# Optimization experiments

Measured on AMD Instinct MI355X. Metric: run time of the kernel, lower is better.

## Reference

```python
import jax, jax.numpy as jnp
import numpy as np
from jax import lax

EPS = 1e-5

def _conv(x, w, b, pad):
    y = lax.conv_general_dilated(x, w, (1, 1), [(pad, pad), (pad, pad)],
                                 dimension_numbers=('NCHW', 'OIHW', 'NCHW'))
    return y + b[None, :, None, None]

def _bn(x, g, b, m, v):
    # eval-mode BatchNorm2d with running stats
    scale = g * lax.rsqrt(v + EPS)
    return x * scale[None, :, None, None] + (b - m * scale)[None, :, None, None]

def setup_inputs() -> dict:
    key = jax.random.key(0)
    ks = jax.random.split(key, 16)
    B, C, H, W = 16, 64, 128, 128
    C2 = 2 * C
    d = {}
    d['x'] = jax.random.normal(ks[0], (B, C, H, W), jnp.float32)
    # fc1: Conv2d(C,C,3,p=1) + BN(C)
    d['fc1_w'] = jax.random.normal(ks[1], (C, C, 3, 3), jnp.float32) * 0.05
    d['fc1_b'] = jax.random.normal(ks[2], (C,), jnp.float32) * 0.05
    d['bn1_g'] = jnp.ones((C,), jnp.float32)
    d['bn1_b'] = jnp.zeros((C,), jnp.float32)
    d['bn1_m'] = jax.random.normal(ks[3], (C,), jnp.float32) * 0.05
    d['bn1_v'] = jax.random.uniform(ks[4], (C,), jnp.float32) * 0.5 + 0.5
    # graph_conv.nn: Conv2d(2C,2C,1) + BN(2C) + GELU
    d['gc_w'] = jax.random.normal(ks[5], (C2, C2, 1, 1), jnp.float32) * 0.05
    d['gc_b'] = jax.random.normal(ks[6], (C2,), jnp.float32) * 0.05
    d['bng_g'] = jnp.ones((C2,), jnp.float32)
    d['bng_b'] = jnp.zeros((C2,), jnp.float32)
    d['bng_m'] = jax.random.normal(ks[7], (C2,), jnp.float32) * 0.05
    d['bng_v'] = jax.random.uniform(ks[8], (C2,), jnp.float32) * 0.5 + 0.5
    # fc2: Conv2d(2C,C,3,p=1) + BN(C)
    d['fc2_w'] = jax.random.normal(ks[9], (C, C2, 3, 3), jnp.float32) * 0.05
    d['fc2_b'] = jax.random.normal(ks[10], (C,), jnp.float32) * 0.05
    d['bn2_g'] = jnp.ones((C,), jnp.float32)
    d['bn2_b'] = jnp.zeros((C,), jnp.float32)
    d['bn2_m'] = jax.random.normal(ks[11], (C,), jnp.float32) * 0.05
    d['bn2_v'] = jax.random.uniform(ks[12], (C,), jnp.float32) * 0.5 + 0.5
    return d

def reference(x, fc1_w, fc1_b, bn1_g, bn1_b, bn1_m, bn1_v,
              gc_w, gc_b, bng_g, bng_b, bng_m, bng_v,
              fc2_w, fc2_b, bn2_g, bn2_b, bn2_m, bn2_v):
    # fc1
    h = _bn(_conv(x, fc1_w, fc1_b, 1), bn1_g, bn1_b, bn1_m, bn1_v)
    # MRConv4dSP: strided self-attention over superpatch tokens
    sel = h[:, :, ::4, ::4]                          # [B,C,h4,w4]
    B, C, h4, w4 = sel.shape
    q = sel.reshape(B, C, h4 * w4).transpose(0, 2, 1)  # [B,N,C]
    scale = C ** (-0.5)
    att = jax.nn.softmax(jnp.einsum('bnc,bmc->bnm', q, q) * scale, axis=-1)
    o = jnp.einsum('bnm,bmc->bnc', att, q)           # [B,N,C]
    o = o.transpose(0, 2, 1).reshape(B, C, h4, w4)
    o = jnp.repeat(jnp.repeat(o, 4, axis=2), 4, axis=3)
    g = jnp.concatenate([h, o], axis=1)              # [B,2C,H,W]
    g = jax.nn.gelu(_bn(_conv(g, gc_w, gc_b, 0), bng_g, bng_b, bng_m, bng_v),
                    approximate=False)
    # fc2 + residual (drop_path=0 -> identity)
    y = _bn(_conv(g, fc2_w, fc2_b, 1), bn2_g, bn2_b, bn2_m, bn2_v)
    return y + x
```

## Files before the change

### kernel.cpp

```cpp
#include <hip/hip_runtime.h>
#include <math.h>

#define EPSV 1e-5f

typedef __bf16 bf16;
using bf16x8 = __attribute__((ext_vector_type(8))) __bf16;
using bf16x4 = __attribute__((ext_vector_type(4))) __bf16;
using bf16x2 = __attribute__((ext_vector_type(2))) __bf16;
using f32x4  = __attribute__((ext_vector_type(4))) float;

static __device__ __forceinline__ f32x4 mfma16(bf16x8 a, bf16x8 b, f32x4 c) {
    return __builtin_amdgcn_mfma_f32_16x16x32_bf16(a, b, c, 0, 0, 0);
}
static __device__ __forceinline__ f32x4 zero4() {
    f32x4 z = {0.f, 0.f, 0.f, 0.f};
    return z;
}

typedef __attribute__((address_space(1))) const char g_char_t;
typedef __attribute__((address_space(3))) char lds_char_t;
static __device__ __forceinline__ void gll16(const void* g, void* l) {
    __builtin_amdgcn_global_load_lds((g_char_t*)g, (lds_char_t*)l, 16, 0, 0);
}

static __device__ __forceinline__ float gelu_f(float v) {
    float z = fabsf(v) * 0.70710678118f;
    float t = __builtin_amdgcn_rcpf(1.f + 0.3275911f * z);
    float poly = t * (0.254829592f + t * (-0.284496736f + t * (1.421413741f +
                 t * (-1.453152027f + t * 1.061405429f))));
    float e = __expf(-z * z);
    float erfv = copysignf(1.f - poly * e, v);
    return 0.5f * v * (1.f + erfv);
}

static __device__ __forceinline__ void prep3x3_one(const float* w, bf16* wt,
                                                   int t, int CIN)
{
    int cout = t / CIN, ci = t - cout * CIN;
    int cci = ci >> 5, lg = (ci >> 3) & 3, j = ci & 7;
    int mi = cout >> 4, lix = cout & 15;
#pragma unroll
    for (int kgt = 0; kgt < 9; ++kgt) {
        float v = w[(size_t)t * 9 + kgt];
        wt[((((size_t)kgt * (CIN >> 5) + cci) * 4 + mi) * 64 + lg * 16 + lix) * 8 + j]
            = (bf16)v;
    }
}

__global__ __launch_bounds__(256) void prep_cvt(
    const float* __restrict__ x, bf16* __restrict__ xb,
    const float* __restrict__ fc1_w, const float* __restrict__ fc2_w,
    const float* __restrict__ gc_w,
    bf16* __restrict__ wt1, bf16* __restrict__ wt2, bf16* __restrict__ wtg,
    float* __restrict__ zb)
{
    __shared__ float t_lds[64 * 68];
    const int bx = blockIdx.x, tid = threadIdx.x;
    if (bx < 4096) {
        const int b = bx >> 8, inner = bx & 255;
        const int y = inner >> 1, x0 = (inner & 1) * 64;
        for (int f = tid; f < 64 * 16; f += 256) {
            int c = f >> 4, xu = f & 15;
            float4 v = *(const float4*)&x[((size_t)(b * 64 + c) << 14) + (y << 7) + x0 + xu * 4];
            t_lds[(xu * 4 + 0) * 68 + c] = v.x;
            t_lds[(xu * 4 + 1) * 68 + c] = v.y;
            t_lds[(xu * 4 + 2) * 68 + c] = v.z;
            t_lds[(xu * 4 + 3) * 68 + c] = v.w;
        }
        __syncthreads();
        for (int f = tid; f < 64 * 8; f += 256) {
            int xx = f >> 3, cu = f & 7;
            const float* p = &t_lds[xx * 68 + cu * 8];
            bf16x8 v;
#pragma unroll
            for (int j = 0; j < 8; ++j) v[j] = (bf16)p[j];
            *(bf16x8*)&xb[((size_t)((b * 128 + y) * 128) + x0 + xx) * 64 + cu * 8] = v;
        }
    } else {
        int px = bx - 4096;
        if (px < 16) {
            prep3x3_one(fc1_w, wt1, px * 256 + tid, 64);
        } else if (px < 48) {
            prep3x3_one(fc2_w, wt2, (px - 16) * 256 + tid, 128);
        } else {
            if (px == 48 && tid < 64)
                ((float4*)zb)[tid] = make_float4(0.f, 0.f, 0.f, 0.f);
            int t = (px - 48) * 256 + tid;
            int cout = t >> 7, ci = t & 127;
            int ks = ci >> 5, lg = (ci >> 3) & 3, j = ci & 7;
            wtg[(((size_t)(ks * 4 + lg) * 128) + cout) * 8 + j] = (bf16)gc_w[t];
        }
    }
}

template<int CIN, int OUTMODE>
__global__ __launch_bounds__(512) void conv3x3_mfma(
    const bf16* __restrict__ in, const bf16* __restrict__ wt,
    const float* __restrict__ bias,
    const float* __restrict__ bg, const float* __restrict__ bb,
    const float* __restrict__ bm, const float* __restrict__ bv,
    const bf16* __restrict__ resid, const bf16* __restrict__ zb,
    void* __restrict__ outp, bf16* __restrict__ qout)
{
    constexpr int NC = CIN >> 5;
    __shared__ bf16 in_lds[2][672 * 32];
    __shared__ bf16 w_lds[2][36 * 512];

    const int wg = blockIdx.x;
    const int v  = (wg & 7) * 64 + (wg >> 3);
    const int tile = v & 31, b = v >> 5;
    const int x0 = (tile & 1) * 64;
    const int y0 = (tile >> 1) * 8;
    const int tid  = threadIdx.x;
    const int wid  = tid >> 6;
    const int lane = tid & 63;
    const int lix  = lane & 15, lg = lane >> 4;

    int goff[6]; bool gok[6];
#pragma unroll
    for (int i = 0; i < 6; ++i) {
        int chunk = wid + 8 * i;
        int f = chunk * 64 + lane;
        int pix = f >> 2, u = f & 3;
        int sw = (pix & 3) ^ ((pix >> 2) & 3);
        int ug = u ^ sw;
        int iy = pix / 66, ix = pix - iy * 66;
        int gy = y0 + iy - 1, gx = x0 + ix - 1;
        gok[i]  = (chunk < 42) && (pix < 660) &&
                  (unsigned)gy < 128u && (unsigned)gx < 128u;
        goff[i] = ((b * 128 + gy) * 128 + gx) * CIN + ug * 8;
    }
    int rd[9];
#pragma unroll
    for (int kg = 0; kg < 3; ++kg)
#pragma unroll
        for (int t = 0; t < 3; ++t) {
            int pix0 = (wid + kg) * 66 + lix + t;
            int sw = (pix0 & 3) ^ ((pix0 >> 2) & 3);
            rd[kg * 3 + t] = pix0 * 32 + ((lg ^ sw) << 3);
        }

    f32x4 acc[4][4];
#pragma unroll
    for (int i = 0; i < 4; ++i)
#pragma unroll
        for (int j = 0; j < 4; ++j) acc[i][j] = zero4();

    auto issue_in = [&](int cci, int buf) {
#pragma unroll
        for (int i = 0; i < 6; ++i) {
            int chunk = wid + 8 * i;
            if (chunk < 42) {
                const void* src = gok[i] ? (const void*)(in + goff[i] + cci * 32)
                                         : (const void*)zb;
                gll16(src, (char*)&in_lds[buf][0] + chunk * 1024);
            }
        }
    };
    auto issue_w = [&](int cci, int buf) {
#pragma unroll
        for (int i = 0; i < 5; ++i) {
            int chunk = wid + 8 * i;
            if (chunk < 36) {
                const bf16* src = wt + ((size_t)(chunk >> 2) * NC + cci) * 2048
                                     + (chunk & 3) * 512 + lane * 8;
                gll16(src, (char*)&w_lds[buf][0] + chunk * 1024);
            }
        }
    };
    auto compute = [&](int buf) {
        bf16x8 afA[4], bfA[4], afB[4], bfB[4];
#pragma unroll
        for (int mi = 0; mi < 4; ++mi)
            afA[mi] = *(const bf16x8*)&w_lds[buf][(0 * 4 + mi) * 512 + lane * 8];
#pragma unroll
        for (int nj = 0; nj < 4; ++nj)
            bfA[nj] = *(const bf16x8*)&in_lds[buf][rd[0] + nj * 512];
#pragma unroll
        for (int kgt = 0; kgt < 9; ++kgt) {
            bf16x8* afC = (kgt & 1) ? afB : afA;
            bf16x8* bfC = (kgt & 1) ? bfB : bfA;
            bf16x8* afN = (kgt & 1) ? afA : afB;
            bf16x8* bfN = (kgt & 1) ? bfA : bfB;
            if (kgt < 8) {
#pragma unroll
                for (int mi = 0; mi < 4; ++mi)
                    afN[mi] = *(const bf16x8*)&w_lds[buf][((kgt + 1) * 4 + mi) * 512 + lane * 8];
#pragma unroll
                for (int nj = 0; nj < 4; ++nj)
                    bfN[nj] = *(const bf16x8*)&in_lds[buf][rd[kgt + 1] + nj * 512];
            }
            __builtin_amdgcn_sched_barrier(0);
#pragma unroll
            for (int nj = 0; nj < 4; ++nj)
#pragma unroll
                for (int mi = 0; mi < 4; ++mi)
                    acc[mi][nj] = mfma16(afC[mi], bfC[nj], acc[mi][nj]);
            __builtin_amdgcn_sched_barrier(0);
        }
    };

    issue_in(0, 0);
    issue_w(0, 0);
#pragma unroll 1
    for (int c = 0; c < NC; ++c) {
        if (c + 1 < NC) {
            issue_in(c + 1, (c + 1) & 1);
            issue_w(c + 1, (c + 1) & 1);
            if (wid < 2)      asm volatile("s_waitcnt vmcnt(11)" ::: "memory");
            else if (wid < 4) asm volatile("s_waitcnt vmcnt(10)" ::: "memory");
            else              asm volatile("s_waitcnt vmcnt(9)"  ::: "memory");
        } else {
            asm volatile("s_waitcnt vmcnt(0)" ::: "memory");
        }
        __builtin_amdgcn_s_barrier();
        __builtin_amdgcn_sched_barrier(0);
        compute(c & 1);
        __builtin_amdgcn_s_barrier();
    }

    if (OUTMODE == 0) {
        bf16* out = (bf16*)outp;
        bf16* stg = &in_lds[0][0];
#pragma unroll
        for (int mi = 0; mi < 4; ++mi) {
            float A[4], Bc[4];
#pragma unroll
            for (int r = 0; r < 4; ++r) {
                int c = mi * 16 + lg * 4 + r;
                float s = bg[c] * rsqrtf(bv[c] + EPSV);
                A[r]  = s;
                Bc[r] = bias[c] * s + bb[c] - bm[c] * s;
            }
#pragma unroll
            for (int nj = 0; nj < 4; ++nj) {
                int px = nj * 16 + lix;
                bf16x4 vv;
#pragma unroll
                for (int r = 0; r < 4; ++r)
                    vv[r] = (bf16)(acc[mi][nj][r] * A[r] + Bc[r]);
                *(bf16x4*)&stg[(wid * 64 + px) * 68 + mi * 16 + lg * 4] = vv;
            }
        }
        __syncthreads();
#pragma unroll
        for (int k = 0; k < 8; ++k) {
            int idx = k * 512 + tid;
            int row = idx >> 9, rem = idx & 511;
            int px = rem >> 3, cu = rem & 7;
            bf16x8 vv = *(const bf16x8*)&stg[(row * 64 + px) * 68 + cu * 8];
            *(bf16x8*)&out[((size_t)((b * 128 + y0 + row) * 128)
                            + x0 + px) * 64 + cu * 8] = vv;
        }
        if (qout && tid < 256) {
            int row4 = (tid >> 7) * 4;
            int rem  = tid & 127;
            int px4  = (rem >> 3) * 4, cu = rem & 7;
            int gy = y0 + row4, gx = x0 + px4;
            int n = ((gy >> 2) << 5) + (gx >> 2);
            bf16x8 vv = *(const bf16x8*)&stg[(row4 * 64 + px4) * 68 + cu * 8];
            *(bf16x8*)&qout[((size_t)(b * 1024 + n)) * 64 + cu * 8] = vv;
        }
    } else {
        float* out = (float*)outp;
        const int gy = y0 + wid;
#pragma unroll
        for (int mi = 0; mi < 4; ++mi) {
            float A[4], Bc[4];
#pragma unroll
            for (int r = 0; r < 4; ++r) {
                int c = mi * 16 + lg * 4 + r;
                float s = bg[c] * rsqrtf(bv[c] + EPSV);
                A[r]  = s;
                Bc[r] = bias[c] * s + bb[c] - bm[c] * s;
            }
#pragma unroll
            for (int nj = 0; nj < 4; ++nj) {
                int px = x0 + nj * 16 + lix;
                bf16x4 rv = *(const bf16x4*)&resid[((size_t)((b * 128 + gy) * 128) + px) * 64
                                                   + mi * 16 + lg * 4];
#pragma unroll
                for (int r = 0; r < 4; ++r) {
                    int c = mi * 16 + lg * 4 + r;
                    size_t oi = ((size_t)(b * 64 + c) << 14) + (gy << 7) + px;
                    out[oi] = acc[mi][nj][r] * A[r] + Bc[r] + (float)rv[r];
                }
            }
        }
    }
}

__global__ __launch_bounds__(256) void attn_fused(
    const bf16* __restrict__ q, const bf16* __restrict__ h,
    const bf16* __restrict__ wtg, const float* __restrict__ bias,
    const float* __restrict__ bg, const float* __restrict__ bb,
    const float* __restrict__ bm, const float* __restrict__ bv,
    bf16* __restrict__ g)
{
    __shared__ __align__(16) char smem[62976];
    bf16* qn = (bf16*)smem;
    bf16* kn = (bf16*)(smem + 9216);
    bf16* vt = (bf16*)(smem + 27648);
    bf16* pl = (bf16*)(smem + 45056);
    float* fac = (float*)(smem + 62464);
    bf16* o_lds = (bf16*)smem;
    bf16* h_lds = (bf16*)(smem + 9216);
    bf16* g_lds = (bf16*)(smem + 25600);

    const int n0 = blockIdx.x * 64, b = blockIdx.y;
    const int tid = threadIdx.x, w = tid >> 6, lane = tid & 63;
    const int lix = lane & 15, lg = lane >> 4;
    const bf16* qb = q + ((size_t)b << 16);

    for (int f = tid; f < 512; f += 256) {
        int row = f >> 3, cu = f & 7;
        *(bf16x8*)&qn[row * 72 + cu * 8] =
            *(const bf16x8*)&qb[(size_t)(n0 + row) * 64 + cu * 8];
    }

    float m_run = -3.0e38f, l_run = 0.f;
    f32x4 oacc[4];
#pragma unroll
    for (int ct = 0; ct < 4; ++ct) oacc[ct] = zero4();

    for (int mt = 0; mt < 1024; mt += 128) {
        __syncthreads();
        for (int f = tid; f < 1024; f += 256) {
            int row = f >> 3, cu = f & 7;
            *(bf16x8*)&kn[row * 72 + cu * 8] =
                *(const bf16x8*)&qb[(size_t)(mt + row) * 64 + cu * 8];
        }
        for (int f = tid; f < 512; f += 256) {
            int mp = f >> 3, cu = f & 7;
            int m = mp * 2;
            bf16x8 a = *(const bf16x8*)&qb[(size_t)(mt + m) * 64 + cu * 8];
            bf16x8 c = *(const bf16x8*)&qb[(size_t)(mt + m + 1) * 64 + cu * 8];
#pragma unroll
            for (int j = 0; j < 8; ++j) {
                bf16x2 pr = {a[j], c[j]};
                *(bf16x2*)&vt[(cu * 8 + j) * 136 + m] = pr;
            }
        }
        __syncthreads();

        bf16x8 bq0 = *(const bf16x8*)&qn[(w * 16 + lix) * 72 + lg * 8];
        bf16x8 bq1 = *(const bf16x8*)&qn[(w * 16 + lix) * 72 + 32 + lg * 8];

        f32x4 s[8];
#pragma unroll
        for (int t = 0; t < 8; ++t) {
            bf16x8 a0 = *(const bf16x8*)&kn[(t * 16 + lix) * 72 + lg * 8];
            bf16x8 a1 = *(const bf16x8*)&kn[(t * 16 + lix) * 72 + 32 + lg * 8];
            s[t] = mfma16(a0, bq0, zero4());
            s[t] = mfma16(a1, bq1, s[t]);
        }

        float mx = -3.0e38f;
#pragma unroll
        for (int t = 0; t < 8; ++t)
#pragma unroll
            for (int r = 0; r < 4; ++r) { s[t][r] *= 0.125f; mx = fmaxf(mx, s[t][r]); }
        mx = fmaxf(mx, __shfl_xor(mx, 16));
        mx = fmaxf(mx, __shfl_xor(mx, 32));
        float m_new = fmaxf(m_run, mx);
        float alpha = __expf(m_run - m_new);

        float psum = 0.f;
#pragma unroll
        for (int t = 0; t < 8; ++t) {
            float p0 = __expf(s[t][0] - m_new), p1 = __expf(s[t][1] - m_new);
            float p2 = __expf(s[t][2] - m_new), p3 = __expf(s[t][3] - m_new);
            psum += (p0 + p1) + (p2 + p3);
            bf16x2 v01 = {(bf16)p0, (bf16)p1};
            bf16x2 v23 = {(bf16)p2, (bf16)p3};
            *(bf16x2*)&pl[w * 2176 + lix * 136 + t * 16 + lg * 4]     = v01;
            *(bf16x2*)&pl[w * 2176 + lix * 136 + t * 16 + lg * 4 + 2] = v23;
        }
        psum += __shfl_xor(psum, 16);
        psum += __shfl_xor(psum, 32);
        l_run = l_run * alpha + psum;
        m_run = m_new;
        if (lg == 0) fac[w * 16 + lix] = alpha;

        float4 a4 = *(const float4*)&fac[w * 16 + lg * 4];
        float aa[4] = {a4.x, a4.y, a4.z, a4.w};
#pragma unroll
        for (int ct = 0; ct < 4; ++ct)
#pragma unroll
            for (int r = 0; r < 4; ++r) oacc[ct][r] *= aa[r];

#pragma unroll
        for (int kk = 0; kk < 4; ++kk) {
            bf16x8 pa = *(const bf16x8*)&pl[w * 2176 + lix * 136 + kk * 32 + lg * 8];
#pragma unroll
            for (int ct = 0; ct < 4; ++ct) {
                bf16x8 bv = *(const bf16x8*)&vt[(ct * 16 + lix) * 136 + kk * 32 + lg * 8];
                oacc[ct] = mfma16(pa, bv, oacc[ct]);
            }
        }
    }

    if (lg == 0) fac[w * 16 + lix] = l_run;
    float4 l4 = *(const float4*)&fac[w * 16 + lg * 4];
    float ll[4] = {1.f / l4.x, 1.f / l4.y, 1.f / l4.z, 1.f / l4.w};

    __syncthreads();
#pragma unroll
    for (int ct = 0; ct < 4; ++ct)
#pragma unroll
        for (int r = 0; r < 4; ++r) {
            int nl = w * 16 + lg * 4 + r;
            o_lds[nl * 72 + ct * 16 + lix] = (bf16)(oacc[ct][r] * ll[r]);
        }
    __syncthreads();

    const int ybase = n0 >> 3;
    const int sxor = (lix >> 2) & 3;

    float A2[2][4], B2[2][4];
#pragma unroll
    for (int mi = 0; mi < 2; ++mi)
#pragma unroll
        for (int r = 0; r < 4; ++r) {
            int c = w * 32 + mi * 16 + lg * 4 + r;
            float s = bg[c] * rsqrtf(bv[c] + EPSV);
            A2[mi][r] = s;
            B2[mi][r] = bias[c] * s + bb[c] - bm[c] * s;
        }

    auto issue_h = [&](int pg, int buf) {
        int y = ybase + (pg >> 1), xg = (pg & 1) * 64;
#pragma unroll
        for (int i = 0; i < 2; ++i) {
            int ch = w * 2 + i;
            int px = ch * 8 + (lane >> 3);
            int cu = lane & 7;
            int cus = cu ^ ((px >> 2) & 3);
            const bf16* src = &h[((size_t)((b * 128 + y) * 128) + xg + px) * 64 + cus * 8];
            gll16(src, (char*)h_lds + buf * 8192 + ch * 1024);
        }
    };

    issue_h(0, 0);
#pragma unroll 1
    for (int pg = 0; pg < 16; ++pg) {
        if (pg < 15) {
            issue_h(pg + 1, (pg + 1) & 1);
            asm volatile("s_waitcnt vmcnt(2)" ::: "memory");
        } else {
            asm volatile("s_waitcnt vmcnt(0)" ::: "memory");
        }
        __builtin_amdgcn_s_barrier();

        const int buf = pg & 1;
        const int nlb = (pg >> 3) * 32 + (pg & 1) * 16 + (lix >> 2);

        f32x4 a2[2][4];
#pragma unroll
        for (int mi = 0; mi < 2; ++mi)
#pragma unroll
            for (int nj = 0; nj < 4; ++nj) a2[mi][nj] = zero4();

#pragma unroll
        for (int ks = 0; ks < 4; ++ks) {
            bf16x8 af0 = *(const bf16x8*)&wtg[(((size_t)(ks * 4 + lg) * 128)
                                               + w * 32 + lix) * 8];
            bf16x8 af1 = *(const bf16x8*)&wtg[(((size_t)(ks * 4 + lg) * 128)
                                               + w * 32 + 16 + lix) * 8];
#pragma unroll
            for (int nj = 0; nj < 4; ++nj) {
                bf16x8 bfv;
                if (ks < 2) {
                    int px = nj * 16 + lix;
                    bfv = *(const bf16x8*)&h_lds[buf * 4096 + px * 64
                                                 + ((ks * 4 + (lg ^ sxor)) << 3)];
                } else {
                    int nl = nlb + nj * 4;
                    bfv = *(const bf16x8*)&o_lds[nl * 72 + (((ks - 2) * 4 + lg) << 3)];
                }
                a2[0][nj] = mfma16(af0, bfv, a2[0][nj]);
                a2[1][nj] = mfma16(af1, bfv, a2[1][nj]);
            }
        }

#pragma unroll
        for (int mi = 0; mi < 2; ++mi)
#pragma unroll
            for (int nj = 0; nj < 4; ++nj) {
                int px = nj * 16 + lix;
                bf16x4 vv;
#pragma unroll
                for (int r = 0; r < 4; ++r)
                    vv[r] = (bf16)gelu_f(a2[mi][nj][r] * A2[mi][r] + B2[mi][r]);
                *(bf16x4*)&g_lds[px * 132 + w * 32 + mi * 16 + lg * 4] = vv;
            }
        __builtin_amdgcn_s_barrier();

        {
            int y = ybase + (pg >> 1), xg = (pg & 1) * 64;
#pragma unroll
            for (int k = 0; k < 4; ++k) {
                int idx = k * 256 + tid;
                int px = idx >> 4, cu = idx & 15;
                bf16x8 vv = *(const bf16x8*)&g_lds[px * 132 + cu * 8];
                *(bf16x8*)&g[((size_t)((b * 128 + y) * 128) + xg + px) * 128 + cu * 8] = vv;
            }
        }
        __builtin_amdgcn_s_barrier();
    }
}

extern "C" void kernel_launch(void* const* d_in, const int* in_sizes, int n_in,
                              void* d_out, int out_size, void* d_ws, size_t ws_size,
                              hipStream_t stream)
{
    const float* x     = (const float*)d_in[0];
    const float* fc1_w = (const float*)d_in[1];
    const float* fc1_b = (const float*)d_in[2];
    const float* bn1_g = (const float*)d_in[3];
    const float* bn1_b = (const float*)d_in[4];
    const float* bn1_m = (const float*)d_in[5];
    const float* bn1_v = (const float*)d_in[6];
    const float* gc_w  = (const float*)d_in[7];
    const float* gc_b  = (const float*)d_in[8];
    const float* bng_g = (const float*)d_in[9];
    const float* bng_b = (const float*)d_in[10];
    const float* bng_m = (const float*)d_in[11];
    const float* bng_v = (const float*)d_in[12];
    const float* fc2_w = (const float*)d_in[13];
    const float* fc2_b = (const float*)d_in[14];
    const float* bn2_g = (const float*)d_in[15];
    const float* bn2_b = (const float*)d_in[16];
    const float* bn2_m = (const float*)d_in[17];
    const float* bn2_v = (const float*)d_in[18];

    char* wsb = (char*)d_ws;
    bf16* x_bf = (bf16*)wsb;
    bf16* h    = (bf16*)(wsb + 33554432);
    bf16* g    = (bf16*)(wsb + 67108864);
    bf16* q    = (bf16*)(wsb + 134217728);
    bf16* wt1  = (bf16*)(wsb + 136314880);
    bf16* wt2  = (bf16*)(wsb + 136388608);
    bf16* wtg  = (bf16*)(wsb + 136536064);
    bf16* zb   = (bf16*)(wsb + 136568832);

    prep_cvt<<<4208, 256, 0, stream>>>(x, x_bf, fc1_w, fc2_w, gc_w,
                                       wt1, wt2, wtg, (float*)zb);

    conv3x3_mfma<64, 0><<<512, 512, 0, stream>>>(
        x_bf, wt1, fc1_b, bn1_g, bn1_b, bn1_m, bn1_v, nullptr, zb, h, q);

    attn_fused<<<dim3(16, 16), 256, 0, stream>>>(
        q, h, wtg, gc_b, bng_g, bng_b, bng_m, bng_v, g);

    conv3x3_mfma<128, 1><<<512, 512, 0, stream>>>(
        g, wt2, fc2_b, bn2_g, bn2_b, bn2_m, bn2_v, x_bf, zb, (float*)d_out, nullptr);
}
```

Before: 173.5 us.

## Split attention keys across two wave teams and widen GC phase to full rows

Doubles the attention block to 512 threads. Two teams of four waves each process half of the 1024 keys with online softmax, and their partial max, sum and output are merged through LDS. The fused 1x1 conv+GELU epilogue now processes full 128-pixel rows with 8 waves, using a wider XOR swizzle on the h tile. The aim is to raise parallelism for a grid of only 256 blocks on a many-CU GPU. In exchange it uses much more LDS per block and adds a cross-team merge step.

```diff
diff --git a/kernel.cpp b/kernel.cpp
--- a/kernel.cpp
+++ b/kernel.cpp
@@ -290,30 +290,28 @@
     }
 }
 
-__global__ __launch_bounds__(256) void attn_fused(
+__global__ __launch_bounds__(512) void attn_fused(
     const bf16* __restrict__ q, const bf16* __restrict__ h,
     const bf16* __restrict__ wtg, const float* __restrict__ bias,
     const float* __restrict__ bg, const float* __restrict__ bb,
     const float* __restrict__ bm, const float* __restrict__ bv,
     bf16* __restrict__ g)
 {
-    __shared__ __align__(16) char smem[62976];
-    bf16* qn = (bf16*)smem;
-    bf16* kn = (bf16*)(smem + 9216);
-    bf16* vt = (bf16*)(smem + 27648);
-    bf16* pl = (bf16*)(smem + 45056);
-    float* fac = (float*)(smem + 62464);
-    bf16* o_lds = (bf16*)smem;
-    bf16* h_lds = (bf16*)(smem + 9216);
-    bf16* g_lds = (bf16*)(smem + 25600);
-
+    __shared__ __align__(16) char smem[116224];
     const int n0 = blockIdx.x * 64, b = blockIdx.y;
     const int tid = threadIdx.x, w = tid >> 6, lane = tid & 63;
+    const int wl = w & 3, team = w >> 2, ttid = tid & 255;
     const int lix = lane & 15, lg = lane >> 4;
     const bf16* qb = q + ((size_t)b << 16);
 
-    for (int f = tid; f < 512; f += 256) {
-        int row = f >> 3, cu = f & 7;
+    bf16*  qn  = (bf16*)smem;
+    bf16*  kn  = (bf16*)(smem + 9216 + team * 18432);
+    bf16*  vt  = (bf16*)(smem + 46080 + team * 17408);
+    bf16*  pl  = (bf16*)(smem + 80896 + w * 4352);
+    float* fac = (float*)(smem + 115712 + w * 64);
+
+    {
+        int row = tid >> 3, cu = tid & 7;
         *(bf16x8*)&qn[row * 72 + cu * 8] =
             *(const bf16x8*)&qb[(size_t)(n0 + row) * 64 + cu * 8];
     }
@@ -323,18 +321,20 @@
 #pragma unroll
     for (int ct = 0; ct < 4; ++ct) oacc[ct] = zero4();
 
-    for (int mt = 0; mt < 1024; mt += 128) {
+    const bf16* qteam = qb + ((size_t)team << 9) * 64;
+#pragma unroll 1
+    for (int mt = 0; mt < 512; mt += 128) {
         __syncthreads();
-        for (int f = tid; f < 1024; f += 256) {
+        for (int f = ttid; f < 1024; f += 256) {
             int row = f >> 3, cu = f & 7;
             *(bf16x8*)&kn[row * 72 + cu * 8] =
-                *(const bf16x8*)&qb[(size_t)(mt + row) * 64 + cu * 8];
-        }
-        for (int f = tid; f < 512; f += 256) {
+                *(const bf16x8*)&qteam[(size_t)(mt + row) * 64 + cu * 8];
+        }
+        for (int f = ttid; f < 512; f += 256) {
             int mp = f >> 3, cu = f & 7;
             int m = mp * 2;
-            bf16x8 a = *(const bf16x8*)&qb[(size_t)(mt + m) * 64 + cu * 8];
-            bf16x8 c = *(const bf16x8*)&qb[(size_t)(mt + m + 1) * 64 + cu * 8];
+            bf16x8 a = *(const bf16x8*)&qteam[(size_t)(mt + m) * 64 + cu * 8];
+            bf16x8 c = *(const bf16x8*)&qteam[(size_t)(mt + m + 1) * 64 + cu * 8];
 #pragma unroll
             for (int j = 0; j < 8; ++j) {
                 bf16x2 pr = {a[j], c[j]};
@@ -343,8 +343,8 @@
         }
         __syncthreads();
 
-        bf16x8 bq0 = *(const bf16x8*)&qn[(w * 16 + lix) * 72 + lg * 8];
-        bf16x8 bq1 = *(const bf16x8*)&qn[(w * 16 + lix) * 72 + 32 + lg * 8];
+        bf16x8 bq0 = *(const bf16x8*)&qn[(wl * 16 + lix) * 72 + lg * 8];
+        bf16x8 bq1 = *(const bf16x8*)&qn[(wl * 16 + lix) * 72 + 32 + lg * 8];
 
         f32x4 s[8];
 #pragma unroll
@@ -373,16 +373,16 @@
             psum += (p0 + p1) + (p2 + p3);
             bf16x2 v01 = {(bf16)p0, (bf16)p1};
             bf16x2 v23 = {(bf16)p2, (bf16)p3};
-            *(bf16x2*)&pl[w * 2176 + lix * 136 + t * 16 + lg * 4]     = v01;
-            *(bf16x2*)&pl[w * 2176 + lix * 136 + t * 16 + lg * 4 + 2] = v23;
+            *(bf16x2*)&pl[lix * 136 + t * 16 + lg * 4]     = v01;
+            *(bf16x2*)&pl[lix * 136 + t * 16 + lg * 4 + 2] = v23;
         }
         psum += __shfl_xor(psum, 16);
         psum += __shfl_xor(psum, 32);
         l_run = l_run * alpha + psum;
         m_run = m_new;
-        if (lg == 0) fac[w * 16 + lix] = alpha;
-
-        float4 a4 = *(const float4*)&fac[w * 16 + lg * 4];
+        if (lg == 0) fac[lix] = alpha;
+
+        float4 a4 = *(const float4*)&fac[lg * 4];
         float aa[4] = {a4.x, a4.y, a4.z, a4.w};
 #pragma unroll
         for (int ct = 0; ct < 4; ++ct)
@@ -391,7 +391,7 @@
 
 #pragma unroll
         for (int kk = 0; kk < 4; ++kk) {
-            bf16x8 pa = *(const bf16x8*)&pl[w * 2176 + lix * 136 + kk * 32 + lg * 8];
+            bf16x8 pa = *(const bf16x8*)&pl[lix * 136 + kk * 32 + lg * 8];
 #pragma unroll
             for (int ct = 0; ct < 4; ++ct) {
                 bf16x8 bv = *(const bf16x8*)&vt[(ct * 16 + lix) * 136 + kk * 32 + lg * 8];
@@ -400,51 +400,89 @@
         }
     }
 
-    if (lg == 0) fac[w * 16 + lix] = l_run;
-    float4 l4 = *(const float4*)&fac[w * 16 + lg * 4];
-    float ll[4] = {1.f / l4.x, 1.f / l4.y, 1.f / l4.z, 1.f / l4.w};
-
     __syncthreads();
-#pragma unroll
-    for (int ct = 0; ct < 4; ++ct)
+    float* o1  = (float*)smem;
+    float* m0l = (float*)(smem + 16384);
+    float* l0l = m0l + 64;
+    float* m1l = m0l + 128;
+    float* l1l = m0l + 192;
+    bf16*  o_lds = (bf16*)(smem + 17408);
+
+    if (lg == 0) {
+        if (team == 0) { m0l[wl * 16 + lix] = m_run; l0l[wl * 16 + lix] = l_run; }
+        else           { m1l[wl * 16 + lix] = m_run; l1l[wl * 16 + lix] = l_run; }
+    }
+    if (team == 1) {
+#pragma unroll
+        for (int ct = 0; ct < 4; ++ct)
+#pragma unroll
+            for (int r = 0; r < 4; ++r)
+                o1[(wl * 16 + lg * 4 + r) * 64 + ct * 16 + lix] = oacc[ct][r];
+    }
+    __syncthreads();
+    if (team == 0) {
+        float4 m0v = *(const float4*)&m0l[wl * 16 + lg * 4];
+        float4 l0v = *(const float4*)&l0l[wl * 16 + lg * 4];
+        float4 m1v = *(const float4*)&m1l[wl * 16 + lg * 4];
+        float4 l1v = *(const float4*)&l1l[wl * 16 + lg * 4];
+        float m0a[4] = {m0v.x, m0v.y, m0v.z, m0v.w};
+        float l0a[4] = {l0v.x, l0v.y, l0v.z, l0v.w};
+        float m1a[4] = {m1v.x, m1v.y, m1v.z, m1v.w};
+        float l1a[4] = {l1v.x, l1v.y, l1v.z, l1v.w};
+        float a0[4], a1[4], inv[4];
 #pragma unroll
         for (int r = 0; r < 4; ++r) {
-            int nl = w * 16 + lg * 4 + r;
-            o_lds[nl * 72 + ct * 16 + lix] = (bf16)(oacc[ct][r] * ll[r]);
-        }
+            float mm = fmaxf(m0a[r], m1a[r]);
+            a0[r] = __expf(m0a[r] - mm);
+            a1[r] = __expf(m1a[r] - mm);
+            inv[r] = 1.f / (l0a[r] * a0[r] + l1a[r] * a1[r]);
+        }
+#pragma unroll
+        for (int ct = 0; ct < 4; ++ct)
+#pragma unroll
+            for (int r = 0; r < 4; ++r) {
+                int nl = wl * 16 + lg * 4 + r;
+                float ov = o1[nl * 64 + ct * 16 + lix];
+                o_lds[nl * 72 + ct * 16 + lix] =
+                    (bf16)((oacc[ct][r] * a0[r] + ov * a1[r]) * inv[r]);
+            }
+    }
     __syncthreads();
 
     const int ybase = n0 >> 3;
-    const int sxor = (lix >> 2) & 3;
+    const int wc = w & 3;
+    const int p2 = w >> 2;
+    bf16* h_lds = (bf16*)(smem + 26624);
+    bf16* g_lds = (bf16*)(smem + 59392);
 
     float A2[2][4], B2[2][4];
 #pragma unroll
     for (int mi = 0; mi < 2; ++mi)
 #pragma unroll
         for (int r = 0; r < 4; ++r) {
-            int c = w * 32 + mi * 16 + lg * 4 + r;
+            int c = wc * 32 + mi * 16 + lg * 4 + r;
             float s = bg[c] * rsqrtf(bv[c] + EPSV);
             A2[mi][r] = s;
             B2[mi][r] = bias[c] * s + bb[c] - bm[c] * s;
         }
 
     auto issue_h = [&](int pg, int buf) {
-        int y = ybase + (pg >> 1), xg = (pg & 1) * 64;
+        int y = ybase + pg;
 #pragma unroll
         for (int i = 0; i < 2; ++i) {
             int ch = w * 2 + i;
             int px = ch * 8 + (lane >> 3);
             int cu = lane & 7;
-            int cus = cu ^ ((px >> 2) & 3);
-            const bf16* src = &h[((size_t)((b * 128 + y) * 128) + xg + px) * 64 + cus * 8];
-            gll16(src, (char*)h_lds + buf * 8192 + ch * 1024);
+            int cus = cu ^ (px & 7);
+            const bf16* src = &h[((size_t)((b * 128 + y) * 128) + px) * 64 + cus * 8];
+            gll16(src, (char*)h_lds + buf * 16384 + ch * 1024);
         }
     };
 
     issue_h(0, 0);
 #pragma unroll 1
-    for (int pg = 0; pg < 16; ++pg) {
-        if (pg < 15) {
+    for (int pg = 0; pg < 8; ++pg) {
+        if (pg < 7) {
             issue_h(pg + 1, (pg + 1) & 1);
             asm volatile("s_waitcnt vmcnt(2)" ::: "memory");
         } else {
@@ -453,7 +491,7 @@
         __builtin_amdgcn_s_barrier();
 
         const int buf = pg & 1;
-        const int nlb = (pg >> 3) * 32 + (pg & 1) * 16 + (lix >> 2);
+        const int nlb = (pg >> 2) * 32 + p2 * 16 + (lix >> 2);
 
         f32x4 a2[2][4];
 #pragma unroll
@@ -464,16 +502,16 @@
 #pragma unroll
         for (int ks = 0; ks < 4; ++ks) {
             bf16x8 af0 = *(const bf16x8*)&wtg[(((size_t)(ks * 4 + lg) * 128)
-                                               + w * 32 + lix) * 8];
+                                               + wc * 32 + lix) * 8];
             bf16x8 af1 = *(const bf16x8*)&wtg[(((size_t)(ks * 4 + lg) * 128)
-                                               + w * 32 + 16 + lix) * 8];
+                                               + wc * 32 + 16 + lix) * 8];
 #pragma unroll
             for (int nj = 0; nj < 4; ++nj) {
                 bf16x8 bfv;
                 if (ks < 2) {
-                    int px = nj * 16 + lix;
-                    bfv = *(const bf16x8*)&h_lds[buf * 4096 + px * 64
-                                                 + ((ks * 4 + (lg ^ sxor)) << 3)];
+                    int px = p2 * 64 + nj * 16 + lix;
+                    int slot = (ks * 4 + lg) ^ (px & 7);
+                    bfv = *(const bf16x8*)&h_lds[buf * 8192 + px * 64 + slot * 8];
                 } else {
                     int nl = nlb + nj * 4;
                     bfv = *(const bf16x8*)&o_lds[nl * 72 + (((ks - 2) * 4 + lg) << 3)];
@@ -487,23 +525,23 @@
         for (int mi = 0; mi < 2; ++mi)
 #pragma unroll
             for (int nj = 0; nj < 4; ++nj) {
-                int px = nj * 16 + lix;
+                int px = p2 * 64 + nj * 16 + lix;
                 bf16x4 vv;
 #pragma unroll
                 for (int r = 0; r < 4; ++r)
                     vv[r] = (bf16)gelu_f(a2[mi][nj][r] * A2[mi][r] + B2[mi][r]);
-                *(bf16x4*)&g_lds[px * 132 + w * 32 + mi * 16 + lg * 4] = vv;
+                *(bf16x4*)&g_lds[px * 132 + wc * 32 + mi * 16 + lg * 4] = vv;
             }
         __builtin_amdgcn_s_barrier();
 
         {
-            int y = ybase + (pg >> 1), xg = (pg & 1) * 64;
+            int y = ybase + pg;
 #pragma unroll
             for (int k = 0; k < 4; ++k) {
-                int idx = k * 256 + tid;
+                int idx = k * 512 + tid;
                 int px = idx >> 4, cu = idx & 15;
                 bf16x8 vv = *(const bf16x8*)&g_lds[px * 132 + cu * 8];
-                *(bf16x8*)&g[((size_t)((b * 128 + y) * 128) + xg + px) * 128 + cu * 8] = vv;
+                *(bf16x8*)&g[((size_t)((b * 128 + y) * 128) + px) * 128 + cu * 8] = vv;
             }
         }
         __builtin_amdgcn_s_barrier();
@@ -550,7 +588,7 @@
     conv3x3_mfma<64, 0><<<512, 512, 0, stream>>>(
         x_bf, wt1, fc1_b, bn1_g, bn1_b, bn1_m, bn1_v, nullptr, zb, h, q);
 
-    attn_fused<<<dim3(16, 16), 256, 0, stream>>>(
+    attn_fused<<<dim3(16, 16), 512, 0, stream>>>(
         q, h, wtg, gc_b, bng_g, bng_b, bng_m, bng_v, g);
 
     conv3x3_mfma<128, 1><<<512, 512, 0, stream>>>(
```

Result: faster. 159.4 us (-8.1%).
